# Kernel optimization log

Hardware: AMD Instinct MI355X
Metric: run time of the kernel (lower is better)

The kernel has to match this reference:

```python
import jax, jax.numpy as jnp
import numpy as np

P, L, D, H, K = 128, 800, 200, 100, 2  # passages, seq_len, input dim, hidden, spans per passage
VOCAB = 30522


def setup_inputs() -> dict:
    key = jax.random.key(0)
    ks = jax.random.split(key, 8)
    S_p = jax.random.normal(ks[0], (P, L, D), dtype=jnp.float32)
    # sorted along last axis so start <= end
    spans = jnp.sort(jax.random.randint(ks[1], (P, K, 2), 0, L), axis=-1)
    passages = jax.random.randint(ks[2], (P, L), 0, VOCAB)
    s = 0.05
    Wb = jax.random.normal(ks[3], (H, D), jnp.float32) * s
    We = jax.random.normal(ks[4], (H, D), jnp.float32) * s
    Wc = jax.random.normal(ks[5], (H, H), jnp.float32) * s
    Wo = jax.random.normal(ks[6], (H, H), jnp.float32) * s
    Wv = jax.random.normal(ks[7], (1, H), jnp.float32) * s
    return {"S_p": S_p, "spans": spans, "passages": passages,
            "Wb": Wb, "We": We, "Wc": Wc, "Wo": Wo, "Wv": Wv}


def reference(S_p, spans, passages, Wb, We, Wc, Wo, Wv):
    M = P * K
    p_idx = jnp.repeat(jnp.arange(P), K)            # [M] passage index per candidate
    starts = spans[:, :, 0].reshape(M)
    ends = spans[:, :, 1].reshape(M)
    t = jnp.arange(L)

    # S_Cs: candidate kept at its original position, zero elsewhere (== F.pad of the slice)
    span_mask = (t[None, :] >= starts[:, None]) & (t[None, :] <= ends[:, None])  # [M, L]
    S_Cs = S_p[p_idx] * span_mask[..., None].astype(S_p.dtype)                   # [M, L, D]

    # encoded candidates: token ids shifted to position 0, right-padded with 0
    gidx = jnp.clip(starts[:, None] + t[None, :], 0, L - 1)                      # [M, L]
    len_mask = t[None, :] <= (ends - starts)[:, None]
    encoded_candidates = jnp.where(len_mask, passages[p_idx[:, None], gidx], 0)  # [M, L]

    # condensed representation from start/end token states
    sb = S_p[p_idx, starts]                          # [M, D]
    se = S_p[p_idx, ends]                            # [M, D]
    r_Cs = jnp.tanh(sb @ Wb.T + se @ We.T)           # [M, H]

    # pairwise scores V_full[i, j] = Wv tanh(Wc r_i + Wo r_j)
    c = r_Cs @ Wc.T                                  # [M, H]
    o = r_Cs @ Wo.T                                  # [M, H]
    V_full = jnp.tanh(c[:, None, :] + o[None, :, :]) @ Wv[0]   # [M, M]

    # leave-one-out gather: V[i] = V_full[i, j != i]
    cols = jnp.arange(M - 1)
    rows = jnp.arange(M)
    idx = cols[None, :] + (cols[None, :] >= rows[:, None]).astype(cols.dtype)    # [M, M-1]
    V = V_full[rows[:, None], idx]                   # [M, M-1]

    # alpha[i] = exp(V[i]) / sum_{j != i} exp(V[j])  (per-column, non-standard normalization)
    E = jnp.exp(V)                                   # [M, M-1]
    denom = E.sum(axis=0, keepdims=True) - E
    alpha = E / denom                                # [M, M-1]

    # tilda_r[i] = sum over rows of (alpha excl row i) @ (r_Cs excl row i)
    s_rows = alpha.sum(axis=0, keepdims=True) - alpha   # [M, M-1]
    R_excl = r_Cs[idx]                                  # [M, M-1, H]
    tilda_r_Cs = jnp.einsum('mb,mbh->mh', s_rows, R_excl)  # [M, H]

    return S_Cs, r_Cs, encoded_candidates, V, tilda_r_Cs
```

## Files before the change

### kernel.cpp

```cpp
#include <hip/hip_runtime.h>
#include <math.h>

#define LP 800
#define DP 200
#define HP 100
#define MP 256
#define MM1 255

typedef float fx4 __attribute__((ext_vector_type(4)));

#define OFF_SCS  0u
#define OFF_R    40960000u
#define OFF_ENC  40985600u
#define OFF_V    41190400u
#define OFF_TIL  41255680u

#define WS_C     0u
#define WS_O     25600u
#define WS_S     51200u

#define SCS_TOTAL 5120
#define N3_STREAMERS 1792

__device__ __forceinline__ float tanh_fast(float x) {
    float e = __expf(2.0f * x);
    return 1.0f - 2.0f / (e + 1.0f);
}

__device__ __forceinline__ void scs_slice(const fx4* __restrict__ Sp4,
                                          const int* __restrict__ spans,
                                          fx4* __restrict__ out4,
                                          unsigned sid) {
    unsigned m     = sid / 20u;
    unsigned chunk = sid - m * 20u;
    unsigned p = m >> 1, k = m & 1;
    int start = spans[p * 4 + k * 2];
    int end   = spans[p * 4 + k * 2 + 1];
    const fx4* __restrict__ src = Sp4 + (size_t)p * 40000u;
    fx4* __restrict__ dst       = out4 + (size_t)m * 40000u;
    unsigned base = chunk * 2048u + threadIdx.x;

    if (chunk < 19u) {
        fx4 v[8];
        #pragma unroll
        for (int it = 0; it < 8; ++it) {
            unsigned off = base + (unsigned)it * 256u;
            int t = (int)(off / 50u);
            fx4 x = (fx4)(0.f);
            if (t >= start && t <= end) x = src[off];
            v[it] = x;
        }
        #pragma unroll
        for (int it = 0; it < 8; ++it) {
            unsigned off = base + (unsigned)it * 256u;
            dst[off] = v[it];
        }
    } else {
        #pragma unroll
        for (int it = 0; it < 8; ++it) {
            unsigned off = base + (unsigned)it * 256u;
            if (off < 40000u) {
                int t = (int)(off / 50u);
                fx4 x = (fx4)(0.f);
                if (t >= start && t <= end) x = src[off];
                dst[off] = x;
            }
        }
    }
}

__global__ __launch_bounds__(256) void node1_kernel(const float* __restrict__ Sp,
                                                    const int* __restrict__ spans,
                                                    const int* __restrict__ passages,
                                                    const float* __restrict__ Wb,
                                                    const float* __restrict__ We,
                                                    const float* __restrict__ Wc,
                                                    const float* __restrict__ Wo,
                                                    float* __restrict__ enc,
                                                    float* __restrict__ r_out,
                                                    float* __restrict__ c_ws,
                                                    float* __restrict__ o_ws) {
    __shared__ float4 sb4[50], se4[50], rs4[25];
    int m = blockIdx.x;
    int p = m >> 1, k = m & 1;
    int start = spans[p * 4 + k * 2];
    int end   = spans[p * 4 + k * 2 + 1];
    int tid = threadIdx.x;

    int len = end - start;
    for (int t = tid; t < LP; t += 256) {
        int g = start + t; if (g > LP - 1) g = LP - 1;
        enc[m * LP + t] = (t <= len) ? (float)passages[p * LP + g] : 0.f;
    }

    const float4* sbp = (const float4*)(Sp + (size_t)(p * LP + start) * DP);
    const float4* sep = (const float4*)(Sp + (size_t)(p * LP + end) * DP);
    if (tid < 50)       sb4[tid]      = sbp[tid];
    else if (tid < 100) se4[tid - 50] = sep[tid - 50];
    __syncthreads();

    int h = tid;
    if (h < HP) {
        const float4* wb = (const float4*)(Wb + h * DP);
        const float4* we = (const float4*)(We + h * DP);
        float acc = 0.f;
        #pragma unroll
        for (int d = 0; d < 50; ++d) {
            float4 a = sb4[d], b = wb[d];
            acc += a.x * b.x + a.y * b.y + a.z * b.z + a.w * b.w;
            float4 a2 = se4[d], b2 = we[d];
            acc += a2.x * b2.x + a2.y * b2.y + a2.z * b2.z + a2.w * b2.w;
        }
        float r = tanh_fast(acc);
        ((float*)rs4)[h] = r;
        r_out[m * HP + h] = r;
    }
    __syncthreads();
    if (h < HP) {
        const float4* wc = (const float4*)(Wc + h * HP);
        const float4* wo = (const float4*)(Wo + h * HP);
        float accc = 0.f, acco = 0.f;
        #pragma unroll
        for (int q = 0; q < 25; ++q) {
            float4 r = rs4[q], cc = wc[q], oo = wo[q];
            accc += r.x * cc.x + r.y * cc.y + r.z * cc.z + r.w * cc.w;
            acco += r.x * oo.x + r.y * oo.y + r.z * oo.z + r.w * oo.w;
        }
        c_ws[m * HP + h] = accc;
        o_ws[m * HP + h] = acco;
    }
}

__global__ __launch_bounds__(256) void node2_kernel(const float* __restrict__ c_ws,
                                                    const float* __restrict__ o_ws,
                                                    const float* __restrict__ Wv,
                                                    float* __restrict__ V_out,
                                                    float* __restrict__ s_ws) {
    __shared__ float4 olo4[25], ohi4[25], wv4[25];
    __shared__ float part[4];
    int jp = blockIdx.x;
    int i = threadIdx.x;
    if (i < 25) {
        olo4[i] = ((const float4*)(o_ws + jp * HP))[i];
        ohi4[i] = ((const float4*)(o_ws + (jp + 1) * HP))[i];
        wv4[i]  = ((const float4*)Wv)[i];
    }
    __syncthreads();

    const float4* c4p = (const float4*)(c_ws + i * HP);
    bool hi = (jp >= i);
    float acc = 0.f;
    #pragma unroll
    for (int q = 0; q < 25; ++q) {
        float4 c4 = c4p[q];
        float4 o4 = hi ? ohi4[q] : olo4[q];
        float4 w4 = wv4[q];
        acc += tanh_fast(c4.x + o4.x) * w4.x;
        acc += tanh_fast(c4.y + o4.y) * w4.y;
        acc += tanh_fast(c4.z + o4.z) * w4.z;
        acc += tanh_fast(c4.w + o4.w) * w4.w;
    }
    V_out[i * MM1 + jp] = acc;
    float e = __expf(acc);

    float v = e;
    v += __shfl_down(v, 32); v += __shfl_down(v, 16); v += __shfl_down(v, 8);
    v += __shfl_down(v, 4);  v += __shfl_down(v, 2);  v += __shfl_down(v, 1);
    if ((i & 63) == 0) part[i >> 6] = v;
    __syncthreads();
    float colE = part[0] + part[1] + part[2] + part[3];

    float a = e / (colE - e);

    __syncthreads();
    float v2 = a;
    v2 += __shfl_down(v2, 32); v2 += __shfl_down(v2, 16); v2 += __shfl_down(v2, 8);
    v2 += __shfl_down(v2, 4);  v2 += __shfl_down(v2, 2);  v2 += __shfl_down(v2, 1);
    if ((i & 63) == 0) part[i >> 6] = v2;
    __syncthreads();
    float colA = part[0] + part[1] + part[2] + part[3];

    s_ws[i * MM1 + jp] = colA - a;
}

__global__ __launch_bounds__(256) void node3_kernel(const float* __restrict__ Sp,
                                                    const int* __restrict__ spans,
                                                    const float* __restrict__ s_ws,
                                                    const float* __restrict__ r_out,
                                                    float* __restrict__ til_out,
                                                    fx4* __restrict__ out4) {
    if (blockIdx.x >= MP) {
        for (unsigned sid = (unsigned)(blockIdx.x - MP); sid < SCS_TOTAL;
             sid += N3_STREAMERS)
            scs_slice((const fx4*)Sp, spans, out4, sid);
        return;
    }
    __shared__ float s[MM1 + 1];
    int i = blockIdx.x;
    for (int jp = threadIdx.x; jp < MM1; jp += 256)
        s[jp] = s_ws[i * MM1 + jp];
    __syncthreads();
    int h = threadIdx.x;
    if (h < HP) {
        float acc = 0.f;
        #pragma unroll 4
        for (int jp = 0; jp < i; ++jp)
            acc += s[jp] * r_out[jp * HP + h];
        #pragma unroll 4
        for (int jp = i; jp < MM1; ++jp)
            acc += s[jp] * r_out[(jp + 1) * HP + h];
        til_out[i * HP + h] = acc;
    }
}

extern "C" void kernel_launch(void* const* d_in, const int* in_sizes, int n_in,
                              void* d_out, int out_size, void* d_ws, size_t ws_size,
                              hipStream_t stream) {
    const float* S_p      = (const float*)d_in[0];
    const int*   spans    = (const int*)d_in[1];
    const int*   passages = (const int*)d_in[2];
    const float* Wb       = (const float*)d_in[3];
    const float* We       = (const float*)d_in[4];
    const float* Wc       = (const float*)d_in[5];
    const float* Wo       = (const float*)d_in[6];
    const float* Wv       = (const float*)d_in[7];

    float* out = (float*)d_out;
    float* ws  = (float*)d_ws;

    float* out_scs = out + OFF_SCS;
    float* out_r   = out + OFF_R;
    float* out_enc = out + OFF_ENC;
    float* out_v   = out + OFF_V;
    float* out_til = out + OFF_TIL;

    float* ws_c = ws + WS_C;
    float* ws_o = ws + WS_O;
    float* ws_s = ws + WS_S;

    fx4* out4 = (fx4*)out_scs;

    node1_kernel<<<MP, 256, 0, stream>>>(S_p, spans, passages,
                                         Wb, We, Wc, Wo,
                                         out_enc, out_r, ws_c, ws_o);
    node2_kernel<<<MM1, 256, 0, stream>>>(ws_c, ws_o, Wv, out_v, ws_s);
    node3_kernel<<<MP + N3_STREAMERS, 256, 0, stream>>>(S_p, spans, ws_s, out_r,
                                                        out_til, out4);
}
```

Before: 273.4 us.

## Zero S_Cs with memset and copy only span rows inside node1

The S_Cs output is now cleared with hipMemsetAsync, and streaming blocks copy only the in-span rows from S_p, skipping out-of-span slices early. The streaming work moves from node3 into node1 so it can overlap with the candidate encoding compute. This removes the per-element index division and masking, but it writes span regions twice and adds a separate memset pass over the full output.

```diff
diff --git a/kernel.cpp b/kernel.cpp
--- a/kernel.cpp
+++ b/kernel.cpp
@@ -19,52 +19,45 @@
 #define WS_O     25600u
 #define WS_S     51200u
 
-#define SCS_TOTAL 5120
-#define N3_STREAMERS 1792
+#define SCS_SLOTS 5120
+#define N1_STREAMERS 1792
 
 __device__ __forceinline__ float tanh_fast(float x) {
     float e = __expf(2.0f * x);
     return 1.0f - 2.0f / (e + 1.0f);
 }
 
-__device__ __forceinline__ void scs_slice(const fx4* __restrict__ Sp4,
+__device__ __forceinline__ void span_copy(const fx4* __restrict__ Sp4,
                                           const int* __restrict__ spans,
                                           fx4* __restrict__ out4,
                                           unsigned sid) {
-    unsigned m     = sid / 20u;
-    unsigned chunk = sid - m * 20u;
+    unsigned m = sid / 20u;
+    unsigned w = sid - m * 20u;
     unsigned p = m >> 1, k = m & 1;
     int start = spans[p * 4 + k * 2];
     int end   = spans[p * 4 + k * 2 + 1];
+    unsigned s0 = (unsigned)start * 50u;
+    unsigned s1 = (unsigned)(end + 1) * 50u;
+    unsigned w0 = s0 + w * 2048u;
+    if (w0 >= s1) return;
+
     const fx4* __restrict__ src = Sp4 + (size_t)p * 40000u;
     fx4* __restrict__ dst       = out4 + (size_t)m * 40000u;
-    unsigned base = chunk * 2048u + threadIdx.x;
-
-    if (chunk < 19u) {
+    unsigned base = w0 + threadIdx.x;
+
+    if (w0 + 2048u <= s1) {
         fx4 v[8];
+        #pragma unroll
+        for (int it = 0; it < 8; ++it)
+            v[it] = src[base + (unsigned)it * 256u];
+        #pragma unroll
+        for (int it = 0; it < 8; ++it)
+            dst[base + (unsigned)it * 256u] = v[it];
+    } else {
         #pragma unroll
         for (int it = 0; it < 8; ++it) {
             unsigned off = base + (unsigned)it * 256u;
-            int t = (int)(off / 50u);
-            fx4 x = (fx4)(0.f);
-            if (t >= start && t <= end) x = src[off];
-            v[it] = x;
-        }
-        #pragma unroll
-        for (int it = 0; it < 8; ++it) {
-            unsigned off = base + (unsigned)it * 256u;
-            dst[off] = v[it];
-        }
-    } else {
-        #pragma unroll
-        for (int it = 0; it < 8; ++it) {
-            unsigned off = base + (unsigned)it * 256u;
-            if (off < 40000u) {
-                int t = (int)(off / 50u);
-                fx4 x = (fx4)(0.f);
-                if (t >= start && t <= end) x = src[off];
-                dst[off] = x;
-            }
+            if (off < s1) dst[off] = src[off];
         }
     }
 }
@@ -79,7 +72,14 @@
                                                     float* __restrict__ enc,
                                                     float* __restrict__ r_out,
                                                     float* __restrict__ c_ws,
-                                                    float* __restrict__ o_ws) {
+                                                    float* __restrict__ o_ws,
+                                                    fx4* __restrict__ out4) {
+    if (blockIdx.x >= MP) {
+        for (unsigned sid = (unsigned)(blockIdx.x - MP); sid < SCS_SLOTS;
+             sid += N1_STREAMERS)
+            span_copy((const fx4*)Sp, spans, out4, sid);
+        return;
+    }
     __shared__ float4 sb4[50], se4[50], rs4[25];
     int m = blockIdx.x;
     int p = m >> 1, k = m & 1;
@@ -183,18 +183,9 @@
     s_ws[i * MM1 + jp] = colA - a;
 }
 
-__global__ __launch_bounds__(256) void node3_kernel(const float* __restrict__ Sp,
-                                                    const int* __restrict__ spans,
-                                                    const float* __restrict__ s_ws,
+__global__ __launch_bounds__(256) void node3_kernel(const float* __restrict__ s_ws,
                                                     const float* __restrict__ r_out,
-                                                    float* __restrict__ til_out,
-                                                    fx4* __restrict__ out4) {
-    if (blockIdx.x >= MP) {
-        for (unsigned sid = (unsigned)(blockIdx.x - MP); sid < SCS_TOTAL;
-             sid += N3_STREAMERS)
-            scs_slice((const fx4*)Sp, spans, out4, sid);
-        return;
-    }
+                                                    float* __restrict__ til_out) {
     __shared__ float s[MM1 + 1];
     int i = blockIdx.x;
     for (int jp = threadIdx.x; jp < MM1; jp += 256)
@@ -240,10 +231,12 @@
 
     fx4* out4 = (fx4*)out_scs;
 
-    node1_kernel<<<MP, 256, 0, stream>>>(S_p, spans, passages,
-                                         Wb, We, Wc, Wo,
-                                         out_enc, out_r, ws_c, ws_o);
+    hipMemsetAsync((void*)out_scs, 0, (size_t)OFF_R * sizeof(float), stream);
+
+    node1_kernel<<<MP + N1_STREAMERS, 256, 0, stream>>>(S_p, spans, passages,
+                                                        Wb, We, Wc, Wo,
+                                                        out_enc, out_r, ws_c, ws_o,
+                                                        out4);
     node2_kernel<<<MM1, 256, 0, stream>>>(ws_c, ws_o, Wv, out_v, ws_s);
-    node3_kernel<<<MP + N3_STREAMERS, 256, 0, stream>>>(S_p, spans, ws_s, out_r,
-                                                        out_til, out4);
-}
+    node3_kernel<<<MP, 256, 0, stream>>>(ws_s, out_r, out_til);
+}
```

Result: slower. 286.4 us (+4.8%).
